# Kernel tuning notes

Measured on AMD Instinct MI355X. Metric: run time of the kernel, lower is better.

## Reference

```python
import jax, jax.numpy as jnp
import numpy as np

N = 100000   # nodes
E = 1600000  # edges
F_IN, H1, H2, C = 22, 128, 256, 4


def spmm(edge_src, edge_dst, edge_w, X):
    # A @ X where A is sparse (COO): out[d] = sum_{e: dst[e]=d} w[e] * X[src[e]]
    msgs = X[edge_src] * edge_w[:, None]          # [E, F]
    return jax.ops.segment_sum(msgs, edge_dst, num_segments=N)


def setup_inputs() -> dict:
    key = jax.random.key(0)
    ks = jax.random.split(key, 10)
    x = jax.random.normal(ks[0], (N, F_IN), dtype=jnp.float32)
    edge_src = jax.random.randint(ks[1], (E,), 0, N, dtype=jnp.int32)
    edge_dst = jax.random.randint(ks[2], (E,), 0, N, dtype=jnp.int32)
    edge_w = jax.random.uniform(ks[3], (E,), dtype=jnp.float32)
    s1 = 1.0 / np.sqrt(H1)
    s2 = 1.0 / np.sqrt(H2)
    W1 = jax.random.uniform(ks[4], (F_IN, H1), jnp.float32, -s1, s1)
    b1 = jax.random.uniform(ks[5], (H1,), jnp.float32, -s1, s1)
    W2 = jax.random.uniform(ks[6], (H1, H2), jnp.float32, -s2, s2)
    b2 = jax.random.uniform(ks[7], (H2,), jnp.float32, -s2, s2)
    Wm = jax.random.normal(ks[8], (H2, C), dtype=jnp.float32) * 0.05
    bm = jnp.zeros((C,), dtype=jnp.float32)
    return {"x": x, "edge_src": edge_src, "edge_dst": edge_dst, "edge_w": edge_w,
            "W1": W1, "b1": b1, "W2": W2, "b2": b2, "Wm": Wm, "bm": bm}


def reference(x, edge_src, edge_dst, edge_w, W1, b1, W2, b2, Wm, bm):
    # Layer 1: relu(A @ (X @ W1) + b1)
    h = jax.nn.relu(spmm(edge_src, edge_dst, edge_w, x @ W1) + b1)
    # dropout is a no-op in eval mode
    # Layer 2: A @ (h @ W2) + b2
    h = spmm(edge_src, edge_dst, edge_w, h @ W2) + b2
    # MLP head: Linear(256,4) + LogSoftmax(dim=1)
    return jax.nn.log_softmax(h @ Wm + bm, axis=-1)
```

## Files before the change

### kernel.cpp

```cpp
#include <hip/hip_runtime.h>

#define N_NODES 100000
#define N_EDGES 1600000
#define F_IN 22
#define H1 128
#define H2 256
#define C_OUT 4

#define WDEC(q) __uint_as_float(((q) & 0x7fffu) << 16)
#define BFLO(u) __uint_as_float((u) << 16)
#define BFHI(u) __uint_as_float((u) & 0xFFFF0000u)

#define BSHIFT 9
#define NBUCK 196
#define CHUNK 4096
#define NBLK_A 391
#define BCAP 12288
#define BSLACK 3584
#define XB_BLOCKS 4297

__global__ __launch_bounds__(256) void binA_xb_k(
    const int* __restrict__ esrc, const int* __restrict__ edst,
    const float* __restrict__ ew, int* __restrict__ bcnt,
    uint2* __restrict__ binned,
    const float* __restrict__ x, unsigned* __restrict__ xb)
{
    __shared__ uint2 l_rec[CHUNK];
    __shared__ int l_base[NBUCK];
    __shared__ int l_cnt[NBUCK];
    int t = threadIdx.x;
    int bid = blockIdx.x;

    if (bid >= NBLK_A) {
        int i = (bid - NBLK_A) * 256 + t;
        if (i < N_NODES * 11) {
            int n = i / 11, p = i - n * 11;
            unsigned u0 = __float_as_uint(x[n * F_IN + 2 * p]);
            unsigned u1 = __float_as_uint(x[n * F_IN + 2 * p + 1]);
            u0 = (u0 + 0x7fffu + ((u0 >> 16) & 1u)) >> 16;
            u1 = (u1 + 0x7fffu + ((u1 >> 16) & 1u)) >> 16;
            xb[i] = u0 | (u1 << 16);
        }
        return;
    }

    int e0 = bid * CHUNK;
    int n = min(CHUNK, N_EDGES - e0);

    for (int i = t; i < NBUCK; i += 256) l_cnt[i] = 0;
    __syncthreads();
    for (int i = t; i < n; i += 256) {
        int e = e0 + i;
        int d = edst[e];
        unsigned u = __float_as_uint(ew[e]);
        unsigned bw = (u + 0x7fffu + ((u >> 16) & 1u)) >> 16;
        unsigned rec = ((unsigned)esrc[e] << 15) | bw;
        l_rec[i] = make_uint2(rec, (unsigned)d);
        atomicAdd(&l_cnt[d >> BSHIFT], 1);
    }
    __syncthreads();
    for (int i = t; i < NBUCK; i += 256) {
        int c = l_cnt[i];
        l_base[i] = c ? atomicAdd(&bcnt[i], c) : 0;
    }
    __syncthreads();
    for (int i = t; i < NBUCK; i += 256) l_cnt[i] = 0;
    __syncthreads();
    for (int i = t; i < n; i += 256) {
        uint2 r = l_rec[i];
        int d = (int)r.y;
        int b = d >> BSHIFT;
        int off = l_base[b] + atomicAdd(&l_cnt[b], 1);
        if (off < BCAP)
            binned[(size_t)b * BCAP + off] = make_uint2(r.x, (unsigned)(d & 511));
    }
}

__global__ __launch_bounds__(512) void scanB_wf_k(
    const int* __restrict__ bcnt, int* __restrict__ bbase,
    const float* __restrict__ W2, const float* __restrict__ Wm,
    const float* __restrict__ b2, const float* __restrict__ bm,
    float* __restrict__ Wf, float* __restrict__ bhead)
{
    int t = threadIdx.x;
    if (blockIdx.x == 0) {
        __shared__ int sA[512], sB[512];
        int v = (t < NBUCK) ? ((bcnt[t] + BSLACK + 7) & ~7) : 0;
        sA[t] = v; __syncthreads();
        int* src = sA; int* dst = sB;
        for (int off = 1; off < 512; off <<= 1) {
            dst[t] = src[t] + (t >= off ? src[t - off] : 0);
            __syncthreads();
            int* tmp = src; src = dst; dst = tmp;
        }
        if (t < NBUCK) bbase[t] = (t > 0) ? src[t - 1] : 0;
    } else {
        int k = t >> 2, c = t & 3;
        float acc = 0.f;
        for (int j = 0; j < H2; ++j)
            acc = fmaf(W2[k * H2 + j], Wm[j * C_OUT + c], acc);
        Wf[k * C_OUT + c] = acc;
        if (t < C_OUT) {
            float a = bm[t];
            for (int j = 0; j < H2; ++j)
                a = fmaf(b2[j], Wm[j * C_OUT + t], a);
            bhead[t] = a;
        }
    }
}

__global__ __launch_bounds__(512) void binB_k(
    const uint2* __restrict__ binned, const int* __restrict__ bcnt,
    const int* __restrict__ bbase, int* __restrict__ rowbeg,
    int* __restrict__ rowend, unsigned* __restrict__ rec_s)
{
    __shared__ int l_hist[512];
    __shared__ int sA[512], sB[512];
    __shared__ int l_cur[512];
    __shared__ unsigned l_out[BCAP];
    int b = blockIdx.x;
    int t = threadIdx.x;
    int node0 = b << BSHIFT;
    int base = bbase[b];
    int cnt = min(bcnt[b], BCAP);
    const uint2* reg = binned + (size_t)b * BCAP;

    l_hist[t] = 0;
    __syncthreads();
    for (int i = t; i < cnt; i += 512)
        atomicAdd(&l_hist[reg[i].y], 1);
    __syncthreads();
    int pc = (l_hist[t] + 7) & ~7;
    sA[t] = pc; __syncthreads();
    int* src = sA; int* dst = sB;
    for (int off = 1; off < 512; off <<= 1) {
        dst[t] = src[t] + (t >= off ? src[t - off] : 0);
        __syncthreads();
        int* tmp = src; src = dst; dst = tmp;
    }
    int excl = (t > 0) ? src[t - 1] : 0;
    int ptot = src[511];
    int node = node0 + t;
    if (node < N_NODES) {
        rowbeg[node] = base + excl;
        rowend[node] = base + excl + pc;
    }
    l_cur[t] = excl;
    __syncthreads();
    for (int i = t; i < ptot; i += 512) l_out[i] = 0;
    __syncthreads();
    for (int i = t; i < cnt; i += 512) {
        uint2 r = reg[i];
        int p = atomicAdd(&l_cur[r.y], 1);
        l_out[p] = r.x;
    }
    __syncthreads();
    for (int i = t; i < ptot; i += 512)
        rec_s[base + i] = l_out[i];
}

__global__ __launch_bounds__(256) void layer1z_k(
    const unsigned* __restrict__ xb,
    const int* __restrict__ rowbeg,
    const int* __restrict__ rowend,
    const unsigned* __restrict__ rec,
    const float* __restrict__ W1,
    const float* __restrict__ b1,
    const float* __restrict__ Wf,
    float4* __restrict__ z)
{
    __shared__ float4 ws1[F_IN * 32];
    __shared__ float4 wsf[H1];
    __shared__ float ys[8][24];
    int tid = threadIdx.x;
    int g = tid >> 5, lane = tid & 31;
    int d = blockIdx.x * 8 + g;
    int beg = rowbeg[d], end = rowend[d];

    for (int i = tid; i < F_IN * 32; i += 256) ws1[i] = ((const float4*)W1)[i];
    if (tid < H1) wsf[tid] = ((const float4*)Wf)[tid];

    int l2 = lane < 22 ? lane : 21;
    int eslot = l2 >= 11;
    int pair = l2 - 11 * eslot;

    float aA0 = 0.f, aA1 = 0.f, aA2 = 0.f, aA3 = 0.f;
    float aB0 = 0.f, aB1 = 0.f, aB2 = 0.f, aB3 = 0.f;
    int j = beg;
    for (; j + 16 <= end; j += 16) {
        const uint4* r4 = (const uint4*)(rec + j + 8 * eslot);
        uint4 qa = r4[0];
        uint4 qb = r4[1];
        unsigned x0 = xb[(size_t)(qa.x >> 15) * 11 + pair];
        unsigned x1 = xb[(size_t)(qa.y >> 15) * 11 + pair];
        unsigned x2 = xb[(size_t)(qa.z >> 15) * 11 + pair];
        unsigned x3 = xb[(size_t)(qa.w >> 15) * 11 + pair];
        unsigned x4 = xb[(size_t)(qb.x >> 15) * 11 + pair];
        unsigned x5 = xb[(size_t)(qb.y >> 15) * 11 + pair];
        unsigned x6 = xb[(size_t)(qb.z >> 15) * 11 + pair];
        unsigned x7 = xb[(size_t)(qb.w >> 15) * 11 + pair];
        float w0 = WDEC(qa.x), w1 = WDEC(qa.y), w2 = WDEC(qa.z), w3 = WDEC(qa.w);
        float w4 = WDEC(qb.x), w5 = WDEC(qb.y), w6 = WDEC(qb.z), w7 = WDEC(qb.w);
        aA0 = fmaf(w0, BFLO(x0), aA0); aB0 = fmaf(w0, BFHI(x0), aB0);
        aA1 = fmaf(w1, BFLO(x1), aA1); aB1 = fmaf(w1, BFHI(x1), aB1);
        aA2 = fmaf(w2, BFLO(x2), aA2); aB2 = fmaf(w2, BFHI(x2), aB2);
        aA3 = fmaf(w3, BFLO(x3), aA3); aB3 = fmaf(w3, BFHI(x3), aB3);
        aA0 = fmaf(w4, BFLO(x4), aA0); aB0 = fmaf(w4, BFHI(x4), aB0);
        aA1 = fmaf(w5, BFLO(x5), aA1); aB1 = fmaf(w5, BFHI(x5), aB1);
        aA2 = fmaf(w6, BFLO(x6), aA2); aB2 = fmaf(w6, BFHI(x6), aB2);
        aA3 = fmaf(w7, BFLO(x7), aA3); aB3 = fmaf(w7, BFHI(x7), aB3);
    }
    if (j < end) {
        const uint4* r4 = (const uint4*)(rec + j + 4 * eslot);
        uint4 q = r4[0];
        unsigned x0 = xb[(size_t)(q.x >> 15) * 11 + pair];
        unsigned x1 = xb[(size_t)(q.y >> 15) * 11 + pair];
        unsigned x2 = xb[(size_t)(q.z >> 15) * 11 + pair];
        unsigned x3 = xb[(size_t)(q.w >> 15) * 11 + pair];
        float w0 = WDEC(q.x), w1 = WDEC(q.y), w2 = WDEC(q.z), w3 = WDEC(q.w);
        aA0 = fmaf(w0, BFLO(x0), aA0); aB0 = fmaf(w0, BFHI(x0), aB0);
        aA1 = fmaf(w1, BFLO(x1), aA1); aB1 = fmaf(w1, BFHI(x1), aB1);
        aA2 = fmaf(w2, BFLO(x2), aA2); aB2 = fmaf(w2, BFHI(x2), aB2);
        aA3 = fmaf(w3, BFLO(x3), aA3); aB3 = fmaf(w3, BFHI(x3), aB3);
    }
    float sA = (aA0 + aA1) + (aA2 + aA3);
    float sB = (aB0 + aB1) + (aB2 + aB3);
    float oA = __shfl(sA, 11 + pair, 32);
    float oB = __shfl(sB, 11 + pair, 32);
    if (lane < 11) {
        ys[g][2 * pair]     = sA + oA;
        ys[g][2 * pair + 1] = sB + oB;
    }
    __syncthreads();

    float4 a = ((const float4*)b1)[lane];
#pragma unroll
    for (int k = 0; k < F_IN; ++k) {
        float y = ys[g][k];
        float4 w = ws1[k * 32 + lane];
        a.x = fmaf(y, w.x, a.x);
        a.y = fmaf(y, w.y, a.y);
        a.z = fmaf(y, w.z, a.z);
        a.w = fmaf(y, w.w, a.w);
    }
    a.x = a.x > 0.f ? a.x : 0.f;
    a.y = a.y > 0.f ? a.y : 0.f;
    a.z = a.z > 0.f ? a.z : 0.f;
    a.w = a.w > 0.f ? a.w : 0.f;

    float av[4] = {a.x, a.y, a.z, a.w};
    float pl[4] = {0.f, 0.f, 0.f, 0.f};
#pragma unroll
    for (int r = 0; r < 4; ++r) {
        float4 w = wsf[lane * 4 + r];
        pl[0] = fmaf(av[r], w.x, pl[0]);
        pl[1] = fmaf(av[r], w.y, pl[1]);
        pl[2] = fmaf(av[r], w.z, pl[2]);
        pl[3] = fmaf(av[r], w.w, pl[3]);
    }
#pragma unroll
    for (int mask = 16; mask >= 1; mask >>= 1) {
#pragma unroll
        for (int c = 0; c < 4; ++c)
            pl[c] += __shfl_xor(pl[c], mask, 64);
    }
    if (lane == 0)
        z[d] = make_float4(pl[0], pl[1], pl[2], pl[3]);
}

__global__ __launch_bounds__(256) void agg4_k(
    const float4* __restrict__ z,
    const int* __restrict__ rowbeg,
    const int* __restrict__ rowend,
    const unsigned* __restrict__ rec,
    const float* __restrict__ bhead,
    float* __restrict__ out)
{
    int tid = threadIdx.x;
    int g = tid >> 3, sub = tid & 7;
    int d = blockIdx.x * 32 + g;
    int beg = rowbeg[d], end = rowend[d];

    float4 acc = {0.f, 0.f, 0.f, 0.f};
    for (int j = beg + sub; j < end; j += 8) {
        unsigned r = rec[j];
        float w = WDEC(r);
        float4 v = z[r >> 15];
        acc.x = fmaf(w, v.x, acc.x);
        acc.y = fmaf(w, v.y, acc.y);
        acc.z = fmaf(w, v.z, acc.z);
        acc.w = fmaf(w, v.w, acc.w);
    }
#pragma unroll
    for (int mask = 4; mask >= 1; mask >>= 1) {
        acc.x += __shfl_xor(acc.x, mask, 64);
        acc.y += __shfl_xor(acc.y, mask, 64);
        acc.z += __shfl_xor(acc.z, mask, 64);
        acc.w += __shfl_xor(acc.w, mask, 64);
    }
    if (sub == 0) {
        float l0 = acc.x + bhead[0];
        float l1 = acc.y + bhead[1];
        float l2 = acc.z + bhead[2];
        float l3 = acc.w + bhead[3];
        float mx = fmaxf(fmaxf(l0, l1), fmaxf(l2, l3));
        float s = expf(l0 - mx) + expf(l1 - mx) + expf(l2 - mx) + expf(l3 - mx);
        float lg = mx + logf(s);
        ((float4*)out)[d] = make_float4(l0 - lg, l1 - lg, l2 - lg, l3 - lg);
    }
}

extern "C" void kernel_launch(void* const* d_in, const int* in_sizes, int n_in,
                              void* d_out, int out_size, void* d_ws, size_t ws_size,
                              hipStream_t stream) {
    const float* x    = (const float*)d_in[0];
    const int*   esrc = (const int*)d_in[1];
    const int*   edst = (const int*)d_in[2];
    const float* ew   = (const float*)d_in[3];
    const float* W1   = (const float*)d_in[4];
    const float* b1   = (const float*)d_in[5];
    const float* W2   = (const float*)d_in[6];
    const float* b2   = (const float*)d_in[7];
    const float* Wm   = (const float*)d_in[8];
    const float* bm   = (const float*)d_in[9];
    float* out = (float*)d_out;

    char* ws = (char*)d_ws;
    float4*   z      = (float4*)ws;   ws += (size_t)N_NODES * 16;
    uint2*    binned = (uint2*)ws;    ws += (size_t)NBUCK * BCAP * 8;
    unsigned* rec_s  = (unsigned*)ws; ws += (size_t)(N_EDGES + NBUCK * (BSLACK + 8)) * 4;
    unsigned* xb     = (unsigned*)ws; ws += (size_t)N_NODES * 11 * 4;
    int*      rowbeg = (int*)ws;      ws += (size_t)N_NODES * 4;
    int*      rowend = (int*)ws;      ws += (size_t)N_NODES * 4;
    int*      bcnt   = (int*)ws;      ws += NBUCK * 4;
    int*      bbase  = (int*)ws;      ws += NBUCK * 4;
    float*    Wf     = (float*)ws;    ws += H1 * C_OUT * 4;
    float*    bhead  = (float*)ws;    ws += C_OUT * 4;

    hipMemsetAsync(bcnt, 0, NBUCK * 4, stream);
    binA_xb_k<<<NBLK_A + XB_BLOCKS, 256, 0, stream>>>(
        esrc, edst, ew, bcnt, binned, x, xb);

    scanB_wf_k<<<2, 512, 0, stream>>>(bcnt, bbase, W2, Wm, b2, bm, Wf, bhead);

    binB_k<<<NBUCK, 512, 0, stream>>>(binned, bcnt, bbase, rowbeg, rowend, rec_s);

    layer1z_k<<<N_NODES / 8, 256, 0, stream>>>(xb, rowbeg, rowend, rec_s, W1, b1, Wf, z);
    agg4_k<<<N_NODES / 32, 256, 0, stream>>>(z, rowbeg, rowend, rec_s, bhead, out);
}
```

Baseline: 115.7 us.

## Split layer-1 aggregation from dense transform and use bf16 MFMA for X·W1

The fused layer-1 kernel is split in two. The first kernel only aggregates neighbour features and writes them as bf16 into a padded 32-wide buffer. The second kernel runs the 22x128 W1 transform with 16x16x32 bf16 MFMA instructions, then applies bias, ReLU and the folded Wf head projection to produce z. This takes the per-node scalar FMA loop and its block-wide sync out of the latency-bound gather kernel. In exchange it adds an extra launch, a round trip of a 6.4 MB intermediate through memory, and bf16 rounding of the aggregated features and of W1.

```diff
diff --git a/kernel.cpp b/kernel.cpp
--- a/kernel.cpp
+++ b/kernel.cpp
@@ -18,6 +18,9 @@
 #define BCAP 12288
 #define BSLACK 3584
 #define XB_BLOCKS 4297
+
+typedef __attribute__((ext_vector_type(8))) short bf16x8;
+typedef __attribute__((ext_vector_type(4))) float f32x4;
 
 __global__ __launch_bounds__(256) void binA_xb_k(
     const int* __restrict__ esrc, const int* __restrict__ edst,
@@ -159,26 +162,17 @@
         rec_s[base + i] = l_out[i];
 }
 
-__global__ __launch_bounds__(256) void layer1z_k(
+__global__ __launch_bounds__(256) void agg1_k(
     const unsigned* __restrict__ xb,
     const int* __restrict__ rowbeg,
     const int* __restrict__ rowend,
     const unsigned* __restrict__ rec,
-    const float* __restrict__ W1,
-    const float* __restrict__ b1,
-    const float* __restrict__ Wf,
-    float4* __restrict__ z)
-{
-    __shared__ float4 ws1[F_IN * 32];
-    __shared__ float4 wsf[H1];
-    __shared__ float ys[8][24];
+    unsigned* __restrict__ yb)
+{
     int tid = threadIdx.x;
     int g = tid >> 5, lane = tid & 31;
     int d = blockIdx.x * 8 + g;
     int beg = rowbeg[d], end = rowend[d];
-
-    for (int i = tid; i < F_IN * 32; i += 256) ws1[i] = ((const float4*)W1)[i];
-    if (tid < H1) wsf[tid] = ((const float4*)Wf)[tid];
 
     int l2 = lane < 22 ? lane : 21;
     int eslot = l2 >= 11;
@@ -227,45 +221,92 @@
     float sB = (aB0 + aB1) + (aB2 + aB3);
     float oA = __shfl(sA, 11 + pair, 32);
     float oB = __shfl(sB, 11 + pair, 32);
+    unsigned u = 0;
     if (lane < 11) {
-        ys[g][2 * pair]     = sA + oA;
-        ys[g][2 * pair + 1] = sB + oB;
-    }
-    __syncthreads();
-
-    float4 a = ((const float4*)b1)[lane];
-#pragma unroll
-    for (int k = 0; k < F_IN; ++k) {
-        float y = ys[g][k];
-        float4 w = ws1[k * 32 + lane];
-        a.x = fmaf(y, w.x, a.x);
-        a.y = fmaf(y, w.y, a.y);
-        a.z = fmaf(y, w.z, a.z);
-        a.w = fmaf(y, w.w, a.w);
-    }
-    a.x = a.x > 0.f ? a.x : 0.f;
-    a.y = a.y > 0.f ? a.y : 0.f;
-    a.z = a.z > 0.f ? a.z : 0.f;
-    a.w = a.w > 0.f ? a.w : 0.f;
-
-    float av[4] = {a.x, a.y, a.z, a.w};
-    float pl[4] = {0.f, 0.f, 0.f, 0.f};
-#pragma unroll
-    for (int r = 0; r < 4; ++r) {
-        float4 w = wsf[lane * 4 + r];
-        pl[0] = fmaf(av[r], w.x, pl[0]);
-        pl[1] = fmaf(av[r], w.y, pl[1]);
-        pl[2] = fmaf(av[r], w.z, pl[2]);
-        pl[3] = fmaf(av[r], w.w, pl[3]);
-    }
-#pragma unroll
-    for (int mask = 16; mask >= 1; mask >>= 1) {
-#pragma unroll
-        for (int c = 0; c < 4; ++c)
-            pl[c] += __shfl_xor(pl[c], mask, 64);
-    }
-    if (lane == 0)
-        z[d] = make_float4(pl[0], pl[1], pl[2], pl[3]);
+        unsigned ua = __float_as_uint(sA + oA);
+        ua = (ua + 0x7fffu + ((ua >> 16) & 1u)) >> 16;
+        unsigned ub = __float_as_uint(sB + oB);
+        ub = (ub + 0x7fffu + ((ub >> 16) & 1u)) >> 16;
+        u = ua | (ub << 16);
+    }
+    if (lane < 16)
+        yb[(size_t)d * 16 + lane] = u;
+}
+
+__global__ __launch_bounds__(256) void gemmz_k(
+    const unsigned* __restrict__ yb,
+    const float* __restrict__ W1,
+    const float* __restrict__ b1,
+    const float* __restrict__ Wf,
+    float4* __restrict__ z)
+{
+    __shared__ short w1b[8][64][8];
+    __shared__ float4 wsf4[H1];
+    __shared__ float bs[H1];
+    int tid = threadIdx.x;
+
+    for (int idx = tid; idx < 8 * 64 * 8; idx += 256) {
+        int b = idx >> 9;
+        int r = idx & 511;
+        int l = r >> 3, i = r & 7;
+        int k = 8 * (l >> 4) + i;
+        int col = 16 * b + (l & 15);
+        float v = (k < F_IN) ? W1[k * H1 + col] : 0.f;
+        unsigned u = __float_as_uint(v);
+        u = (u + 0x7fffu + ((u >> 16) & 1u)) >> 16;
+        w1b[b][l][i] = (short)u;
+    }
+    if (tid < H1) { wsf4[tid] = ((const float4*)Wf)[tid]; bs[tid] = b1[tid]; }
+    __syncthreads();
+
+    int wid = tid >> 6, lane = tid & 63;
+    int node0 = blockIdx.x * 64 + wid * 16;
+    if (node0 >= N_NODES) return;
+    int row = lane & 15, q = lane >> 4;
+
+    uint4 av = ((const uint4*)yb)[(size_t)(node0 + row) * 4 + q];
+    bf16x8 af = *(bf16x8*)&av;
+
+    float zp[4][4];
+#pragma unroll
+    for (int i = 0; i < 4; ++i)
+#pragma unroll
+        for (int c = 0; c < 4; ++c) zp[i][c] = 0.f;
+
+#pragma unroll
+    for (int b = 0; b < 8; ++b) {
+        bf16x8 bf = *(bf16x8*)&w1b[b][lane][0];
+        f32x4 c = __builtin_amdgcn_mfma_f32_16x16x32_bf16(
+            af, bf, (f32x4){0.f, 0.f, 0.f, 0.f}, 0, 0, 0);
+        int col = 16 * b + (lane & 15);
+        float bias = bs[col];
+        float4 wv = wsf4[col];
+#pragma unroll
+        for (int i = 0; i < 4; ++i) {
+            float v = c[i] + bias;
+            v = v > 0.f ? v : 0.f;
+            zp[i][0] = fmaf(v, wv.x, zp[i][0]);
+            zp[i][1] = fmaf(v, wv.y, zp[i][1]);
+            zp[i][2] = fmaf(v, wv.z, zp[i][2]);
+            zp[i][3] = fmaf(v, wv.w, zp[i][3]);
+        }
+    }
+#pragma unroll
+    for (int mask = 8; mask >= 1; mask >>= 1)
+#pragma unroll
+        for (int i = 0; i < 4; ++i) {
+            zp[i][0] += __shfl_xor(zp[i][0], mask, 64);
+            zp[i][1] += __shfl_xor(zp[i][1], mask, 64);
+            zp[i][2] += __shfl_xor(zp[i][2], mask, 64);
+            zp[i][3] += __shfl_xor(zp[i][3], mask, 64);
+        }
+    if ((lane & 15) == 0) {
+#pragma unroll
+        for (int i = 0; i < 4; ++i) {
+            int n = node0 + 4 * q + i;
+            z[n] = make_float4(zp[i][0], zp[i][1], zp[i][2], zp[i][3]);
+        }
+    }
 }
 
 __global__ __launch_bounds__(256) void agg4_k(
@@ -330,6 +371,7 @@
     uint2*    binned = (uint2*)ws;    ws += (size_t)NBUCK * BCAP * 8;
     unsigned* rec_s  = (unsigned*)ws; ws += (size_t)(N_EDGES + NBUCK * (BSLACK + 8)) * 4;
     unsigned* xb     = (unsigned*)ws; ws += (size_t)N_NODES * 11 * 4;
+    unsigned* yb     = (unsigned*)ws; ws += (size_t)N_NODES * 16 * 4;
     int*      rowbeg = (int*)ws;      ws += (size_t)N_NODES * 4;
     int*      rowend = (int*)ws;      ws += (size_t)N_NODES * 4;
     int*      bcnt   = (int*)ws;      ws += NBUCK * 4;
@@ -345,6 +387,8 @@
 
     binB_k<<<NBUCK, 512, 0, stream>>>(binned, bcnt, bbase, rowbeg, rowend, rec_s);
 
-    layer1z_k<<<N_NODES / 8, 256, 0, stream>>>(xb, rowbeg, rowend, rec_s, W1, b1, Wf, z);
+    agg1_k<<<N_NODES / 8, 256, 0, stream>>>(xb, rowbeg, rowend, rec_s, yb);
+    gemmz_k<<<(N_NODES + 63) / 64, 256, 0, stream>>>(yb, W1, b1, Wf, z);
+
     agg4_k<<<N_NODES / 32, 256, 0, stream>>>(z, rowbeg, rowend, rec_s, bhead, out);
 }
```

Measured after the change: 109.8 us, median of 2. -5.1%, faster.
